# Optimization experiments

Measured on AMD Instinct MI355X. Metric: run time of the kernel, lower is better.

Reference implementation:

```python
import jax, jax.numpy as jnp
import numpy as np

NUM_HEADS = 16

def setup_inputs() -> dict:
    key = jax.random.key(0)
    k1, k2, k3 = jax.random.split(key, 3)
    B, S, D = 2, 2048, 1024
    return {
        "hidden_states": jax.random.normal(k1, (B, S, D), dtype=jnp.float32),
        "W_attn": jax.random.normal(k2, (D, 3 * D), dtype=jnp.float32) * 0.02,
        "b_attn": jnp.zeros((3 * D,), dtype=jnp.float32),
        "W_proj": jax.random.normal(k3, (D, D), dtype=jnp.float32) * 0.02,
        "b_proj": jnp.zeros((D,), dtype=jnp.float32),
    }

def reference(hidden_states, W_attn, b_attn, W_proj, b_proj):
    B, S, D = hidden_states.shape
    H = NUM_HEADS
    hd = D // H
    # qkv projection (Conv1D == addmm): [B,S,3D]
    qkv = hidden_states @ W_attn + b_attn
    q, k, v = jnp.split(qkv, 3, axis=-1)
    # split heads -> [B,H,S,hd]
    def split_heads(t):
        return t.reshape(B, S, H, hd).transpose(0, 2, 1, 3)
    q, k, v = split_heads(q), split_heads(k), split_heads(v)
    # scaled QK^T: [B,H,S,S]
    scores = jnp.einsum('bhqd,bhkd->bhqk', q, k) / jnp.asarray(hd ** 0.5, dtype=q.dtype)
    causal = jnp.tril(jnp.ones((S, S), dtype=bool))
    mask_value = jnp.finfo(scores.dtype).min
    scores = jnp.where(causal, scores, mask_value)
    probs = jax.nn.softmax(scores, axis=-1)  # attn_pdrop=0 -> no dropout
    out = jnp.einsum('bhqk,bhkd->bhqd', probs, v)
    # merge heads -> [B,S,D]
    out = out.transpose(0, 2, 1, 3).reshape(B, S, D)
    out = out @ W_proj + b_proj  # resid_pdrop=0 -> no dropout
    return out
```

## Files before the change

### kernel.cpp

```cpp
#include <hip/hip_runtime.h>
#include <math.h>

typedef __attribute__((ext_vector_type(8))) short bf16x8;
typedef __attribute__((ext_vector_type(4))) short bf16x4;
typedef __attribute__((ext_vector_type(4))) float f32x4;

#define MFMA16(a, b, c) __builtin_amdgcn_mfma_f32_16x16x32_bf16(a, b, c, 0, 0, 0)

#define GLOAD_LDS16(g, l)                                                        \
    __builtin_amdgcn_global_load_lds(                                            \
        (const __attribute__((address_space(1))) void*)(g),                      \
        (__attribute__((address_space(3))) void*)(l), 16, 0, 0)

__device__ __forceinline__ short f2bf(float f) {
    union { float f; unsigned u; } x; x.f = f;
    unsigned r = (x.u + 0x7fffu + ((x.u >> 16) & 1u)) >> 16;
    return (short)r;
}

__global__ __launch_bounds__(256) void convert_bf16_kernel(
    const float* __restrict__ in, short* __restrict__ out, int n4) {
    int i = blockIdx.x * 256 + threadIdx.x;
    if (i >= n4) return;
    float4 v = ((const float4*)in)[i];
    bf16x4 o;
    o[0] = f2bf(v.x); o[1] = f2bf(v.y); o[2] = f2bf(v.z); o[3] = f2bf(v.w);
    ((bf16x4*)out)[i] = o;
}

__global__ __launch_bounds__(256) void transpose_w_kernel(
    const float* __restrict__ W, short* __restrict__ Wt, int K, int N) {
    __shared__ float tile[32][33];
    int c = threadIdx.x & 31, r0 = threadIdx.x >> 5;
    int n0 = blockIdx.x << 5, k0 = blockIdx.y << 5;
#pragma unroll
    for (int i = 0; i < 4; i++) {
        int r = r0 + i * 8;
        tile[r][c] = W[(long)(k0 + r) * N + n0 + c];
    }
    __syncthreads();
#pragma unroll
    for (int i = 0; i < 4; i++) {
        int r = r0 + i * 8;
        Wt[(long)(n0 + r) * K + k0 + c] = f2bf(tile[c][r]);
    }
}

template <int EPI>
__global__ __launch_bounds__(256) void gemm_bt_kernel(
    const short* __restrict__ A, const short* __restrict__ Bt,
    const float* __restrict__ bias, float* __restrict__ outF,
    short* __restrict__ Qb, short* __restrict__ Kb, short* __restrict__ VTb,
    int M, int N, int Kdim) {
    __shared__ __align__(16) short lsA[128 * 64];
    __shared__ __align__(16) short lsB[128 * 64];
    const int tid = threadIdx.x;
    const int lane = tid & 63, l15 = lane & 15, quad = lane >> 4;
    const int w = tid >> 6, wm = w >> 1, wn = w & 1;
    const int m0 = blockIdx.y * 128, n0 = blockIdx.x * 128;
    const int e = l15 & 7;
    const int lrow = lane >> 3;
    const int lgcol = ((lane & 7) ^ lrow) << 3;

    f32x4 acc[4][4];
#pragma unroll
    for (int i = 0; i < 4; i++)
#pragma unroll
        for (int j = 0; j < 4; j++) acc[i][j] = (f32x4){0.f, 0.f, 0.f, 0.f};

    for (int k0 = 0; k0 < Kdim; k0 += 64) {
#pragma unroll
        for (int ii = 0; ii < 4; ii++) {
            const int i = (w << 2) + ii;
            const int grow = (i << 3) + lrow;
            GLOAD_LDS16(&A[(size_t)(m0 + grow) * Kdim + k0 + lgcol], &lsA[i * 512]);
            GLOAD_LDS16(&Bt[(size_t)(n0 + grow) * Kdim + k0 + lgcol], &lsB[i * 512]);
        }
        __syncthreads();
#pragma unroll
        for (int kk = 0; kk < 64; kk += 32) {
            const int kb = kk >> 3;
            bf16x8 af[4], bfr[4];
#pragma unroll
            for (int t = 0; t < 4; t++) {
                const int sw = (((kb + quad) ^ e) << 3);
                af[t] = *(const bf16x8*)&lsA[(wm * 64 + t * 16 + l15) * 64 + sw];
                bfr[t] = *(const bf16x8*)&lsB[(wn * 64 + t * 16 + l15) * 64 + sw];
            }
#pragma unroll
            for (int mt = 0; mt < 4; mt++)
#pragma unroll
                for (int nt = 0; nt < 4; nt++)
                    acc[mt][nt] = MFMA16(af[mt], bfr[nt], acc[mt][nt]);
        }
        __syncthreads();
    }

#pragma unroll
    for (int nt = 0; nt < 4; nt++) {
        int nn = n0 + wn * 64 + nt * 16 + l15;
        float bv = bias[nn];
#pragma unroll
        for (int mt = 0; mt < 4; mt++) {
#pragma unroll
            for (int r = 0; r < 4; r++) {
                int mm = m0 + wm * 64 + mt * 16 + quad * 4 + r;
                float val = acc[mt][nt][r] + bv;
                if (EPI == 0) {
                    outF[(long)mm * N + nn] = val;
                } else {
                    int t = nn >> 10, col = nn & 1023, hh = col >> 6, d = col & 63;
                    int b = mm >> 11, s = mm & 2047;
                    int idx = ((b * 16 + hh) * 2048 + s) * 64 + d;
                    if (t == 0) {
                        Qb[idx] = f2bf(val * 0.18033688011112042f);
                    } else if (t == 1) {
                        Kb[idx] = f2bf(val);
                    } else {
                        VTb[((b * 16 + hh) * 64 + d) * 2048 + s] = f2bf(val);
                    }
                }
            }
        }
    }
}

__global__ __launch_bounds__(256, 4) void attn_kernel(
    const short* __restrict__ Q, const short* __restrict__ Kb,
    const short* __restrict__ VT, short* __restrict__ Ao) {
    __shared__ __align__(16) short Kt[2][64 * 64];
    __shared__ __align__(16) short Vt[2][64 * 64];
    __shared__ __align__(16) short Pt[4][16 * 64];
    const int tid = threadIdx.x;
    const int lane = tid & 63, l15 = lane & 15, quad = lane >> 4, w = tid >> 6;
    const int bx = blockIdx.x;
    const int qt = 31 - (bx >> 5);
    const int hb = bx & 31;
    const int q0 = qt * 64 + w * 16;
    const size_t ho = (size_t)hb * (2048 * 64);
    const short* Qh = Q + ho;
    const short* Kh = Kb + ho;
    const short* Vh = VT + ho;
    short* Pw = &Pt[w][0];
    const int e = l15 & 7;

    const int srow0 = tid >> 3, sc40 = (tid & 7) ^ (srow0 & 7);
    const int srow1 = srow0 + 32, sc41 = (tid & 7) ^ (srow1 & 7);
    const int sdst0 = srow0 * 64 + ((tid & 7) << 3);
    const int sdst1 = srow1 * 64 + ((tid & 7) << 3);

    bf16x8 qf0 = *(const bf16x8*)&Qh[(q0 + l15) * 64 + quad * 8];
    bf16x8 qf1 = *(const bf16x8*)&Qh[(q0 + l15) * 64 + 32 + quad * 8];

    float m = -INFINITY, l = 0.f;
    f32x4 o[4];
#pragma unroll
    for (int dt = 0; dt < 4; dt++) o[dt] = (f32x4){0.f, 0.f, 0.f, 0.f};

    const int nc = qt + 1;

    *(bf16x8*)&Kt[0][sdst0] = *(const bf16x8*)&Kh[srow0 * 64 + sc40 * 8];
    *(bf16x8*)&Kt[0][sdst1] = *(const bf16x8*)&Kh[srow1 * 64 + sc41 * 8];
    *(bf16x8*)&Vt[0][sdst0] = *(const bf16x8*)&Vh[srow0 * 2048 + sc40 * 8];
    *(bf16x8*)&Vt[0][sdst1] = *(const bf16x8*)&Vh[srow1 * 2048 + sc41 * 8];
    __syncthreads();

    for (int c = 0; c < nc; c++) {
        const short* Kc = &Kt[c & 1][0];
        const short* Vc = &Vt[c & 1][0];
        const bool more = (c + 1 < nc);
        bf16x8 kr0, kr1, vr0, vr1;
        if (more) {
            const int k2 = (c + 1) * 64;
            kr0 = *(const bf16x8*)&Kh[(k2 + srow0) * 64 + sc40 * 8];
            kr1 = *(const bf16x8*)&Kh[(k2 + srow1) * 64 + sc41 * 8];
            vr0 = *(const bf16x8*)&Vh[srow0 * 2048 + k2 + sc40 * 8];
            vr1 = *(const bf16x8*)&Vh[srow1 * 2048 + k2 + sc41 * 8];
        }

        f32x4 s[4];
#pragma unroll
        for (int t = 0; t < 4; t++) {
            bf16x8 k0f = *(const bf16x8*)&Kc[(t * 16 + l15) * 64 + ((quad ^ e) << 3)];
            bf16x8 k1f = *(const bf16x8*)&Kc[(t * 16 + l15) * 64 + (((4 + quad) ^ e) << 3)];
            f32x4 z = (f32x4){0.f, 0.f, 0.f, 0.f};
            z = MFMA16(k0f, qf0, z);
            z = MFMA16(k1f, qf1, z);
            s[t] = z;
        }

        if (c == nc - 1) {
#pragma unroll
            for (int t = 0; t < 4; t++)
#pragma unroll
                for (int r = 0; r < 4; r++)
                    if (t * 16 + quad * 4 + r > w * 16 + l15) s[t][r] = -INFINITY;
        }

        float cm = -INFINITY;
#pragma unroll
        for (int t = 0; t < 4; t++)
            cm = fmaxf(cm, fmaxf(fmaxf(s[t][0], s[t][1]), fmaxf(s[t][2], s[t][3])));
        cm = fmaxf(cm, __shfl_xor(cm, 16));
        cm = fmaxf(cm, __shfl_xor(cm, 32));
        const float mn = fmaxf(m, cm);
        const float alpha = __builtin_amdgcn_exp2f(m - mn);
        m = mn;

        float p[4][4];
        float rs = 0.f;
#pragma unroll
        for (int t = 0; t < 4; t++) {
#pragma unroll
            for (int r = 0; r < 4; r++) {
                p[t][r] = __builtin_amdgcn_exp2f(s[t][r] - mn);
                rs += p[t][r];
            }
        }
        rs += __shfl_xor(rs, 16);
        rs += __shfl_xor(rs, 32);
        l = l * alpha + rs;

#pragma unroll
        for (int t = 0; t < 4; t++) {
            bf16x4 pw;
#pragma unroll
            for (int r = 0; r < 4; r++) pw[r] = f2bf(p[t][r]);
            *(bf16x4*)&Pw[l15 * 64 + (((2 * t + (quad >> 1)) ^ e) << 3) + ((quad & 1) << 2)] = pw;
        }

#pragma unroll
        for (int dt = 0; dt < 4; dt++) {
            o[dt][0] *= alpha; o[dt][1] *= alpha; o[dt][2] *= alpha; o[dt][3] *= alpha;
        }

        bf16x8 pf0 = *(const bf16x8*)&Pw[l15 * 64 + ((quad ^ e) << 3)];
        bf16x8 pf1 = *(const bf16x8*)&Pw[l15 * 64 + (((4 + quad) ^ e) << 3)];
#pragma unroll
        for (int dt = 0; dt < 4; dt++) {
            bf16x8 v0f = *(const bf16x8*)&Vc[(dt * 16 + l15) * 64 + ((quad ^ e) << 3)];
            bf16x8 v1f = *(const bf16x8*)&Vc[(dt * 16 + l15) * 64 + (((4 + quad) ^ e) << 3)];
            o[dt] = MFMA16(v0f, pf0, o[dt]);
            o[dt] = MFMA16(v1f, pf1, o[dt]);
        }

        if (more) {
            short* Kn = &Kt[(c + 1) & 1][0];
            short* Vn = &Vt[(c + 1) & 1][0];
            *(bf16x8*)&Kn[sdst0] = kr0;
            *(bf16x8*)&Kn[sdst1] = kr1;
            *(bf16x8*)&Vn[sdst0] = vr0;
            *(bf16x8*)&Vn[sdst1] = vr1;
        }
        __syncthreads();
    }

    const float rl = 1.f / l;
    const int b = hb >> 4, h = hb & 15;
    const long base = ((long)(b * 2048 + q0 + l15)) * 1024 + h * 64;
#pragma unroll
    for (int dt = 0; dt < 4; dt++) {
        bf16x4 wv;
#pragma unroll
        for (int r = 0; r < 4; r++) wv[r] = f2bf(o[dt][r] * rl);
        *(bf16x4*)&Ao[base + dt * 16 + quad * 4] = wv;
    }
}

extern "C" void kernel_launch(void* const* d_in, const int* in_sizes, int n_in,
                              void* d_out, int out_size, void* d_ws, size_t ws_size,
                              hipStream_t stream) {
    const float* hs = (const float*)d_in[0];
    const float* W_attn = (const float*)d_in[1];
    const float* b_attn = (const float*)d_in[2];
    const float* W_proj = (const float*)d_in[3];
    const float* b_proj = (const float*)d_in[4];
    float* out = (float*)d_out;

    char* ws = (char*)d_ws;
    short* hs_bf = (short*)ws;
    short* attn_o = hs_bf;
    short* WaT = (short*)(ws + 8u * 1024 * 1024);
    short* WpT = (short*)(ws + 14u * 1024 * 1024);
    short* Qb = (short*)(ws + 16u * 1024 * 1024);
    short* Kb = (short*)(ws + 24u * 1024 * 1024);
    short* VTb = (short*)(ws + 32u * 1024 * 1024);

    convert_bf16_kernel<<<4096, 256, 0, stream>>>(hs, hs_bf, 1048576);
    transpose_w_kernel<<<dim3(96, 32), 256, 0, stream>>>(W_attn, WaT, 1024, 3072);
    transpose_w_kernel<<<dim3(32, 32), 256, 0, stream>>>(W_proj, WpT, 1024, 1024);
    gemm_bt_kernel<1><<<dim3(24, 32), 256, 0, stream>>>(
        hs_bf, WaT, b_attn, nullptr, Qb, Kb, VTb, 4096, 3072, 1024);
    attn_kernel<<<1024, 256, 0, stream>>>(Qb, Kb, VTb, attn_o);
    gemm_bt_kernel<0><<<dim3(8, 32), 256, 0, stream>>>(
        attn_o, WpT, b_proj, out, nullptr, nullptr, nullptr, 4096, 1024, 1024);
}
```

Measured before the change: 192.4 us.

## Process two query tiles per attention block and restructure QKV epilogue layout

```diff
diff --git a/kernel.cpp b/kernel.cpp
--- a/kernel.cpp
+++ b/kernel.cpp
@@ -28,11 +28,16 @@
     ((bf16x4*)out)[i] = o;
 }
 
-__global__ __launch_bounds__(256) void transpose_w_kernel(
-    const float* __restrict__ W, short* __restrict__ Wt, int K, int N) {
+__global__ __launch_bounds__(256) void transpose_w2_kernel(
+    const float* __restrict__ Wa, const float* __restrict__ Wp,
+    short* __restrict__ WaT, short* __restrict__ WpT) {
     __shared__ float tile[32][33];
+    const float* W; short* Wt; int N, xb;
+    if (blockIdx.x < 96) { W = Wa; Wt = WaT; N = 3072; xb = blockIdx.x; }
+    else                 { W = Wp; Wt = WpT; N = 1024; xb = blockIdx.x - 96; }
+    const int K = 1024;
     int c = threadIdx.x & 31, r0 = threadIdx.x >> 5;
-    int n0 = blockIdx.x << 5, k0 = blockIdx.y << 5;
+    int n0 = xb << 5, k0 = blockIdx.y << 5;
 #pragma unroll
     for (int i = 0; i < 4; i++) {
         int r = r0 + i * 8;
@@ -50,10 +55,11 @@
 __global__ __launch_bounds__(256) void gemm_bt_kernel(
     const short* __restrict__ A, const short* __restrict__ Bt,
     const float* __restrict__ bias, float* __restrict__ outF,
-    short* __restrict__ Qb, short* __restrict__ Kb, short* __restrict__ VTb,
+    short* __restrict__ qkv, short* __restrict__ VTb,
     int M, int N, int Kdim) {
-    __shared__ __align__(16) short lsA[128 * 64];
-    __shared__ __align__(16) short lsB[128 * 64];
+    __shared__ __align__(16) short lsAll[17408];
+    short* lsA = lsAll;
+    short* lsB = lsAll + 8192;
     const int tid = threadIdx.x;
     const int lane = tid & 63, l15 = lane & 15, quad = lane >> 4;
     const int w = tid >> 6, wm = w >> 1, wn = w & 1;
@@ -96,52 +102,76 @@
         __syncthreads();
     }
 
-#pragma unroll
-    for (int nt = 0; nt < 4; nt++) {
-        int nn = n0 + wn * 64 + nt * 16 + l15;
-        float bv = bias[nn];
-#pragma unroll
-        for (int mt = 0; mt < 4; mt++) {
-#pragma unroll
-            for (int r = 0; r < 4; r++) {
-                int mm = m0 + wm * 64 + mt * 16 + quad * 4 + r;
-                float val = acc[mt][nt][r] + bv;
-                if (EPI == 0) {
-                    outF[(long)mm * N + nn] = val;
-                } else {
-                    int t = nn >> 10, col = nn & 1023, hh = col >> 6, d = col & 63;
-                    int b = mm >> 11, s = mm & 2047;
-                    int idx = ((b * 16 + hh) * 2048 + s) * 64 + d;
-                    if (t == 0) {
-                        Qb[idx] = f2bf(val * 0.18033688011112042f);
-                    } else if (t == 1) {
-                        Kb[idx] = f2bf(val);
-                    } else {
-                        VTb[((b * 16 + hh) * 64 + d) * 2048 + s] = f2bf(val);
-                    }
+    if (EPI == 0) {
+#pragma unroll
+        for (int nt = 0; nt < 4; nt++) {
+            int nn = n0 + wn * 64 + nt * 16 + l15;
+            float bv = bias[nn];
+#pragma unroll
+            for (int mt = 0; mt < 4; mt++)
+#pragma unroll
+                for (int r = 0; r < 4; r++) {
+                    int mm = m0 + wm * 64 + mt * 16 + quad * 4 + r;
+                    outF[(long)mm * N + nn] = acc[mt][nt][r] + bv;
                 }
-            }
-        }
-    }
-}
-
-__global__ __launch_bounds__(256, 4) void attn_kernel(
-    const short* __restrict__ Q, const short* __restrict__ Kb,
-    const short* __restrict__ VT, short* __restrict__ Ao) {
+        }
+    } else if (n0 < 2048) {
+        const float scale = (n0 < 1024) ? 0.18033688011112042f : 1.0f;
+#pragma unroll
+        for (int nt = 0; nt < 4; nt++) {
+            int nn = n0 + wn * 64 + nt * 16 + l15;
+            float bv = bias[nn];
+#pragma unroll
+            for (int mt = 0; mt < 4; mt++)
+#pragma unroll
+                for (int r = 0; r < 4; r++) {
+                    int mm = m0 + wm * 64 + mt * 16 + quad * 4 + r;
+                    qkv[(long)mm * 3072 + nn] = f2bf((acc[mt][nt][r] + bv) * scale);
+                }
+        }
+    } else {
+        short* vt = &lsAll[w * (64 * 68)];
+#pragma unroll
+        for (int nt = 0; nt < 4; nt++) {
+            int nn = n0 + wn * 64 + nt * 16 + l15;
+            float bv = bias[nn];
+#pragma unroll
+            for (int mt = 0; mt < 4; mt++) {
+                bf16x4 pk;
+#pragma unroll
+                for (int r = 0; r < 4; r++) pk[r] = f2bf(acc[mt][nt][r] + bv);
+                *(bf16x4*)&vt[(nt * 16 + l15) * 68 + mt * 16 + quad * 4] = pk;
+            }
+        }
+        const int hh = ((n0 - 2048) >> 6) + wn;
+        const int bb = m0 >> 11;
+        const int srow = (m0 & 2047) + wm * 64;
+        const int sloc = (lane & 7) << 3;
+#pragma unroll
+        for (int i = 0; i < 8; i++) {
+            const int d = i * 8 + (lane >> 3);
+            bf16x8 vv = *(const bf16x8*)&vt[d * 68 + sloc];
+            *(bf16x8*)&VTb[((size_t)(bb * 16 + hh) * 64 + d) * 2048 + srow + sloc] = vv;
+        }
+    }
+}
+
+__global__ __launch_bounds__(256, 2) void attn_kernel(
+    const short* __restrict__ qkv, const short* __restrict__ VT,
+    short* __restrict__ Ao) {
     __shared__ __align__(16) short Kt[2][64 * 64];
     __shared__ __align__(16) short Vt[2][64 * 64];
-    __shared__ __align__(16) short Pt[4][16 * 64];
+    __shared__ __align__(16) short Pt[4][2][1024];
     const int tid = threadIdx.x;
     const int lane = tid & 63, l15 = lane & 15, quad = lane >> 4, w = tid >> 6;
     const int bx = blockIdx.x;
-    const int qt = 31 - (bx >> 5);
+    const int qt = 15 - (bx >> 5);
     const int hb = bx & 31;
-    const int q0 = qt * 64 + w * 16;
-    const size_t ho = (size_t)hb * (2048 * 64);
-    const short* Qh = Q + ho;
-    const short* Kh = Kb + ho;
-    const short* Vh = VT + ho;
-    short* Pw = &Pt[w][0];
+    const int b = hb >> 4, h = hb & 15;
+    const size_t rowbase = (size_t)b * 2048 * 3072 + h * 64;
+    const short* Qb = qkv + rowbase;
+    const short* Kb = qkv + rowbase + 1024;
+    const short* Vh = VT + (size_t)hb * 64 * 2048;
     const int e = l15 & 7;
 
     const int srow0 = tid >> 3, sc40 = (tid & 7) ^ (srow0 & 7);
@@ -149,18 +179,25 @@
     const int sdst0 = srow0 * 64 + ((tid & 7) << 3);
     const int sdst1 = srow1 * 64 + ((tid & 7) << 3);
 
-    bf16x8 qf0 = *(const bf16x8*)&Qh[(q0 + l15) * 64 + quad * 8];
-    bf16x8 qf1 = *(const bf16x8*)&Qh[(q0 + l15) * 64 + 32 + quad * 8];
-
-    float m = -INFINITY, l = 0.f;
-    f32x4 o[4];
-#pragma unroll
-    for (int dt = 0; dt < 4; dt++) o[dt] = (f32x4){0.f, 0.f, 0.f, 0.f};
-
-    const int nc = qt + 1;
-
-    *(bf16x8*)&Kt[0][sdst0] = *(const bf16x8*)&Kh[srow0 * 64 + sc40 * 8];
-    *(bf16x8*)&Kt[0][sdst1] = *(const bf16x8*)&Kh[srow1 * 64 + sc41 * 8];
+    bf16x8 qf[2][2];
+#pragma unroll
+    for (int j = 0; j < 2; j++) {
+        const long qr = (long)(qt * 128 + j * 64 + w * 16 + l15) * 3072;
+        qf[j][0] = *(const bf16x8*)&Qb[qr + quad * 8];
+        qf[j][1] = *(const bf16x8*)&Qb[qr + 32 + quad * 8];
+    }
+
+    float m[2] = {-INFINITY, -INFINITY}, l[2] = {0.f, 0.f};
+    f32x4 o[2][4];
+#pragma unroll
+    for (int j = 0; j < 2; j++)
+#pragma unroll
+        for (int dt = 0; dt < 4; dt++) o[j][dt] = (f32x4){0.f, 0.f, 0.f, 0.f};
+
+    const int nc = 2 * qt + 2;
+
+    *(bf16x8*)&Kt[0][sdst0] = *(const bf16x8*)&Kb[(size_t)srow0 * 3072 + sc40 * 8];
+    *(bf16x8*)&Kt[0][sdst1] = *(const bf16x8*)&Kb[(size_t)srow1 * 3072 + sc41 * 8];
     *(bf16x8*)&Vt[0][sdst0] = *(const bf16x8*)&Vh[srow0 * 2048 + sc40 * 8];
     *(bf16x8*)&Vt[0][sdst1] = *(const bf16x8*)&Vh[srow1 * 2048 + sc41 * 8];
     __syncthreads();
@@ -172,76 +209,91 @@
         bf16x8 kr0, kr1, vr0, vr1;
         if (more) {
             const int k2 = (c + 1) * 64;
-            kr0 = *(const bf16x8*)&Kh[(k2 + srow0) * 64 + sc40 * 8];
-            kr1 = *(const bf16x8*)&Kh[(k2 + srow1) * 64 + sc41 * 8];
+            kr0 = *(const bf16x8*)&Kb[(size_t)(k2 + srow0) * 3072 + sc40 * 8];
+            kr1 = *(const bf16x8*)&Kb[(size_t)(k2 + srow1) * 3072 + sc41 * 8];
             vr0 = *(const bf16x8*)&Vh[srow0 * 2048 + k2 + sc40 * 8];
             vr1 = *(const bf16x8*)&Vh[srow1 * 2048 + k2 + sc41 * 8];
         }
 
-        f32x4 s[4];
+        bf16x8 k0f[4], k1f[4];
 #pragma unroll
         for (int t = 0; t < 4; t++) {
-            bf16x8 k0f = *(const bf16x8*)&Kc[(t * 16 + l15) * 64 + ((quad ^ e) << 3)];
-            bf16x8 k1f = *(const bf16x8*)&Kc[(t * 16 + l15) * 64 + (((4 + quad) ^ e) << 3)];
-            f32x4 z = (f32x4){0.f, 0.f, 0.f, 0.f};
-            z = MFMA16(k0f, qf0, z);
-            z = MFMA16(k1f, qf1, z);
-            s[t] = z;
-        }
-
-        if (c == nc - 1) {
+            k0f[t] = *(const bf16x8*)&Kc[(t * 16 + l15) * 64 + ((quad ^ e) << 3)];
+            k1f[t] = *(const bf16x8*)&Kc[(t * 16 + l15) * 64 + (((4 + quad) ^ e) << 3)];
+        }
+
+        float alpha[2];
+        bool act[2];
+#pragma unroll
+        for (int j = 0; j < 2; j++) {
+            act[j] = (c <= 2 * qt + j);
+            alpha[j] = 1.f;
+            if (!act[j]) continue;
+            f32x4 s[4];
+#pragma unroll
+            for (int t = 0; t < 4; t++) {
+                f32x4 z = (f32x4){0.f, 0.f, 0.f, 0.f};
+                z = MFMA16(k0f[t], qf[j][0], z);
+                z = MFMA16(k1f[t], qf[j][1], z);
+                s[t] = z;
+            }
+            if (c == 2 * qt + j) {
+#pragma unroll
+                for (int t = 0; t < 4; t++)
+#pragma unroll
+                    for (int r = 0; r < 4; r++)
+                        if (t * 16 + quad * 4 + r > w * 16 + l15) s[t][r] = -INFINITY;
+            }
+            float cm = -INFINITY;
 #pragma unroll
             for (int t = 0; t < 4; t++)
-#pragma unroll
-                for (int r = 0; r < 4; r++)
-                    if (t * 16 + quad * 4 + r > w * 16 + l15) s[t][r] = -INFINITY;
-        }
-
-        float cm = -INFINITY;
-#pragma unroll
-        for (int t = 0; t < 4; t++)
-            cm = fmaxf(cm, fmaxf(fmaxf(s[t][0], s[t][1]), fmaxf(s[t][2], s[t][3])));
-        cm = fmaxf(cm, __shfl_xor(cm, 16));
-        cm = fmaxf(cm, __shfl_xor(cm, 32));
-        const float mn = fmaxf(m, cm);
-        const float alpha = __builtin_amdgcn_exp2f(m - mn);
-        m = mn;
-
-        float p[4][4];
-        float rs = 0.f;
-#pragma unroll
-        for (int t = 0; t < 4; t++) {
-#pragma unroll
-            for (int r = 0; r < 4; r++) {
-                p[t][r] = __builtin_amdgcn_exp2f(s[t][r] - mn);
-                rs += p[t][r];
-            }
-        }
-        rs += __shfl_xor(rs, 16);
-        rs += __shfl_xor(rs, 32);
-        l = l * alpha + rs;
-
-#pragma unroll
-        for (int t = 0; t < 4; t++) {
-            bf16x4 pw;
-#pragma unroll
-            for (int r = 0; r < 4; r++) pw[r] = f2bf(p[t][r]);
-            *(bf16x4*)&Pw[l15 * 64 + (((2 * t + (quad >> 1)) ^ e) << 3) + ((quad & 1) << 2)] = pw;
-        }
-
-#pragma unroll
-        for (int dt = 0; dt < 4; dt++) {
-            o[dt][0] *= alpha; o[dt][1] *= alpha; o[dt][2] *= alpha; o[dt][3] *= alpha;
-        }
-
-        bf16x8 pf0 = *(const bf16x8*)&Pw[l15 * 64 + ((quad ^ e) << 3)];
-        bf16x8 pf1 = *(const bf16x8*)&Pw[l15 * 64 + (((4 + quad) ^ e) << 3)];
+                cm = fmaxf(cm, fmaxf(fmaxf(s[t][0], s[t][1]), fmaxf(s[t][2], s[t][3])));
+            cm = fmaxf(cm, __shfl_xor(cm, 16));
+            cm = fmaxf(cm, __shfl_xor(cm, 32));
+            const float mn = fmaxf(m[j], cm);
+            alpha[j] = __builtin_amdgcn_exp2f(m[j] - mn);
+            m[j] = mn;
+            float rs = 0.f;
+            short* Pw = &Pt[w][j][0];
+#pragma unroll
+            for (int t = 0; t < 4; t++) {
+                bf16x4 pw;
+#pragma unroll
+                for (int r = 0; r < 4; r++) {
+                    float pv = __builtin_amdgcn_exp2f(s[t][r] - mn);
+                    rs += pv;
+                    pw[r] = f2bf(pv);
+                }
+                *(bf16x4*)&Pw[l15 * 64 + (((2 * t + (quad >> 1)) ^ e) << 3) + ((quad & 1) << 2)] = pw;
+            }
+            rs += __shfl_xor(rs, 16);
+            rs += __shfl_xor(rs, 32);
+            l[j] = l[j] * alpha[j] + rs;
+#pragma unroll
+            for (int dt = 0; dt < 4; dt++) {
+                o[j][dt][0] *= alpha[j]; o[j][dt][1] *= alpha[j];
+                o[j][dt][2] *= alpha[j]; o[j][dt][3] *= alpha[j];
+            }
+        }
+
+        bf16x8 pf0[2], pf1[2];
+#pragma unroll
+        for (int j = 0; j < 2; j++) {
+            if (!act[j]) continue;
+            const short* Pw = &Pt[w][j][0];
+            pf0[j] = *(const bf16x8*)&Pw[l15 * 64 + ((quad ^ e) << 3)];
+            pf1[j] = *(const bf16x8*)&Pw[l15 * 64 + (((4 + quad) ^ e) << 3)];
+        }
 #pragma unroll
         for (int dt = 0; dt < 4; dt++) {
             bf16x8 v0f = *(const bf16x8*)&Vc[(dt * 16 + l15) * 64 + ((quad ^ e) << 3)];
             bf16x8 v1f = *(const bf16x8*)&Vc[(dt * 16 + l15) * 64 + (((4 + quad) ^ e) << 3)];
-            o[dt] = MFMA16(v0f, pf0, o[dt]);
-            o[dt] = MFMA16(v1f, pf1, o[dt]);
+#pragma unroll
+            for (int j = 0; j < 2; j++) {
+                if (!act[j]) continue;
+                o[j][dt] = MFMA16(v0f, pf0[j], o[j][dt]);
+                o[j][dt] = MFMA16(v1f, pf1[j], o[j][dt]);
+            }
         }
 
         if (more) {
@@ -255,15 +307,18 @@
         __syncthreads();
     }
 
-    const float rl = 1.f / l;
-    const int b = hb >> 4, h = hb & 15;
-    const long base = ((long)(b * 2048 + q0 + l15)) * 1024 + h * 64;
-#pragma unroll
-    for (int dt = 0; dt < 4; dt++) {
-        bf16x4 wv;
-#pragma unroll
-        for (int r = 0; r < 4; r++) wv[r] = f2bf(o[dt][r] * rl);
-        *(bf16x4*)&Ao[base + dt * 16 + quad * 4] = wv;
+#pragma unroll
+    for (int j = 0; j < 2; j++) {
+        const float rl = 1.f / l[j];
+        const int qs = qt * 128 + j * 64 + w * 16 + l15;
+        const long base = ((long)(b * 2048 + qs)) * 1024 + h * 64;
+#pragma unroll
+        for (int dt = 0; dt < 4; dt++) {
+            bf16x4 wv;
+#pragma unroll
+            for (int r = 0; r < 4; r++) wv[r] = f2bf(o[j][dt][r] * rl);
+            *(bf16x4*)&Ao[base + dt * 16 + quad * 4] = wv;
+        }
     }
 }
 
@@ -282,16 +337,14 @@
     short* attn_o = hs_bf;
     short* WaT = (short*)(ws + 8u * 1024 * 1024);
     short* WpT = (short*)(ws + 14u * 1024 * 1024);
-    short* Qb = (short*)(ws + 16u * 1024 * 1024);
-    short* Kb = (short*)(ws + 24u * 1024 * 1024);
-    short* VTb = (short*)(ws + 32u * 1024 * 1024);
+    short* qkv = (short*)(ws + 16u * 1024 * 1024);
+    short* VTb = (short*)(ws + 40u * 1024 * 1024);
 
     convert_bf16_kernel<<<4096, 256, 0, stream>>>(hs, hs_bf, 1048576);
-    transpose_w_kernel<<<dim3(96, 32), 256, 0, stream>>>(W_attn, WaT, 1024, 3072);
-    transpose_w_kernel<<<dim3(32, 32), 256, 0, stream>>>(W_proj, WpT, 1024, 1024);
+    transpose_w2_kernel<<<dim3(128, 32), 256, 0, stream>>>(W_attn, W_proj, WaT, WpT);
     gemm_bt_kernel<1><<<dim3(24, 32), 256, 0, stream>>>(
-        hs_bf, WaT, b_attn, nullptr, Qb, Kb, VTb, 4096, 3072, 1024);
-    attn_kernel<<<1024, 256, 0, stream>>>(Qb, Kb, VTb, attn_o);
+        hs_bf, WaT, b_attn, nullptr, qkv, VTb, 4096, 3072, 1024);
+    attn_kernel<<<512, 256, 0, stream>>>(qkv, VTb, attn_o);
     gemm_bt_kernel<0><<<dim3(8, 32), 256, 0, stream>>>(
-        attn_o, WpT, b_proj, out, nullptr, nullptr, nullptr, 4096, 1024, 1024);
-}
+        attn_o, WpT, b_proj, out, nullptr, nullptr, 4096, 1024, 1024);
+}
```

After: 210.7 us. 1.09x slower.
